# Optimization experiments

Measured on AMD Instinct MI355X. Metric: run time of the kernel, lower is better.

## Reference

```python
import jax, jax.numpy as jnp
import numpy as np

BN_EPS = 1e-5

def conv1x1(x, w, b):
    # x: [B,C,H,W], w: [O,C], b: [O] -> [B,O,H,W]
    return jnp.einsum('bchw,oc->bohw', x, w) + b[None, :, None, None]

def setup_inputs() -> dict:
    key = jax.random.key(0)
    ks = jax.random.split(key, 12)
    B, C, H, W = 16, 256, 64, 32
    Ci = C // 2  # reduc_ratio = 2
    s_in = 1.0 / np.sqrt(C)
    s_ci = 1.0 / np.sqrt(Ci)
    return {
        'x':        jax.random.normal(ks[0], (B, C, H, W), jnp.float32),
        'w_theta':  jax.random.normal(ks[1], (Ci, C), jnp.float32) * s_in,
        'b_theta':  jax.random.normal(ks[2], (Ci,), jnp.float32) * 0.01,
        'w_phi':    jax.random.normal(ks[3], (Ci, C), jnp.float32) * s_in,
        'b_phi':    jax.random.normal(ks[4], (Ci,), jnp.float32) * 0.01,
        'w_g':      jax.random.normal(ks[5], (Ci, C), jnp.float32) * s_in,
        'b_g':      jax.random.normal(ks[6], (Ci,), jnp.float32) * 0.01,
        'w_out':    jax.random.normal(ks[7], (C, Ci), jnp.float32) * s_ci,
        'b_out':    jax.random.normal(ks[8], (C,), jnp.float32) * 0.01,
        'gamma':    jax.random.normal(ks[9], (C,), jnp.float32) * 0.1 + 1.0,
        'beta':     jax.random.normal(ks[10], (C,), jnp.float32) * 0.1,
        'run_mean': jax.random.normal(ks[11], (C,), jnp.float32) * 0.1,
        'run_var':  jax.random.uniform(jax.random.fold_in(key, 99), (C,), jnp.float32, 0.5, 1.5),
    }

def reference(x, w_theta, b_theta, w_phi, b_phi, w_g, b_g, w_out, b_out,
              gamma, beta, run_mean, run_var):
    B, C, H, W = x.shape
    Ci = w_theta.shape[0]
    N = H * W
    theta = conv1x1(x, w_theta, b_theta).reshape(B, Ci, N)  # [B,Ci,N]
    phi   = conv1x1(x, w_phi,   b_phi  ).reshape(B, Ci, N)  # [B,Ci,N]
    g     = conv1x1(x, w_g,     b_g    ).reshape(B, Ci, N)  # [B,Ci,N]
    # f = theta^T @ phi, normalized by N (no softmax)
    f = jnp.einsum('bcn,bcm->bnm', theta, phi) / N           # [B,N,N]
    # y = f @ g^T, back to channel-first layout
    y = jnp.einsum('bnm,bcm->bcn', f, g).reshape(B, Ci, H, W)
    w_y = conv1x1(y, w_out, b_out)                           # [B,C,H,W]
    inv = gamma / jnp.sqrt(run_var + BN_EPS)
    bn = w_y * inv[None, :, None, None] + (beta - run_mean * inv)[None, :, None, None]
    return bn + x
```

## Files before the change

kernel.cpp:

```cpp
#include <hip/hip_runtime.h>
#include <cstddef>
#include <cstdint>

typedef unsigned short ushort_t;
typedef short short8 __attribute__((ext_vector_type(8)));
typedef float f32x4 __attribute__((ext_vector_type(4)));

#define BB 16
#define CC 256
#define CI 128
#define KK3 384
#define NN 2048
#define BN_EPS 1e-5f
#define NCHUNK 8

#define OFF_W3H   0u
#define OFF_B3    49152u
#define OFF_B2    49536u
#define OFF_XHT   49792u
#define OFF_THT   4244096u
#define OFF_TPG   6341248u
#define OFF_SPART 10535552u
#define OFF_S     12632704u
#define OFF_MH    12894848u
#define WS_FLOATS 13156992u

__device__ __forceinline__ ushort_t f2bf(float f) {
  unsigned int u = __float_as_uint(f);
  u += 0x7fffu + ((u >> 16) & 1u);
  return (ushort_t)(u >> 16);
}

__device__ __forceinline__ void gl_lds16(const void* gsrc, void* ldst) {
  __builtin_amdgcn_global_load_lds(
      (const __attribute__((address_space(1))) void*)gsrc,
      (__attribute__((address_space(3))) void*)ldst, 16, 0, 0);
}

__device__ __forceinline__ void mfma_core(
    const ushort_t* gA, size_t ldA, const ushort_t* gB, size_t ldB,
    int kIters, ushort_t* ldsA, ushort_t* ldsB, f32x4 acc[4][4]) {
  const int t = threadIdx.x;
  const int wave = t >> 6, lane = t & 63;
  const int wm = wave & 1, wn = wave >> 1;
  const int l15 = lane & 15, lhi = lane >> 4;

  for (int kt = 0; kt < kIters; ++kt) {
#pragma unroll
    for (int q = 0; q < 4; ++q) {
      int row = wave * 32 + q * 8 + (lane >> 3);
      int gs = (lane & 7) ^ (row & 7);
      gl_lds16(gA + (size_t)row * ldA + gs * 8, &ldsA[(wave * 4 + q) * 512]);
    }
#pragma unroll
    for (int q = 0; q < 4; ++q) {
      int row = wave * 32 + q * 8 + (lane >> 3);
      int gs = (lane & 7) ^ (row & 7);
      gl_lds16(gB + (size_t)row * ldB + gs * 8, &ldsB[(wave * 4 + q) * 512]);
    }
    __syncthreads();
#pragma unroll
    for (int ks = 0; ks < 2; ++ks) {
      short8 af[4], bf[4];
#pragma unroll
      for (int i = 0; i < 4; ++i) {
        int rowA = wm * 64 + i * 16 + l15;
        int grA = (4 * ks + lhi) ^ (rowA & 7);
        af[i] = *(const short8*)&ldsA[rowA * 64 + grA * 8];
        int rowB = wn * 64 + i * 16 + l15;
        int grB = (4 * ks + lhi) ^ (rowB & 7);
        bf[i] = *(const short8*)&ldsB[rowB * 64 + grB * 8];
      }
#pragma unroll
      for (int i = 0; i < 4; ++i)
#pragma unroll
        for (int j = 0; j < 4; ++j)
          acc[i][j] = __builtin_amdgcn_mfma_f32_16x16x32_bf16(
              af[i], bf[j], acc[i][j], 0, 0, 0);
    }
    __syncthreads();
    gA += 64; gB += 64;
  }
}

__global__ __launch_bounds__(256) void pack_w(
    const float* __restrict__ wt, const float* __restrict__ bt,
    const float* __restrict__ wp, const float* __restrict__ bp,
    const float* __restrict__ wg, const float* __restrict__ bg,
    const float* __restrict__ b_out, const float* __restrict__ gamma,
    const float* __restrict__ beta, const float* __restrict__ run_mean,
    const float* __restrict__ run_var,
    ushort_t* __restrict__ W3h, float* __restrict__ bias3,
    float* __restrict__ bias2) {
  int gid = blockIdx.x * 256 + threadIdx.x;
  if (gid < KK3 * CC) {
    int k = gid >> 8;
    float v;
    if (k < CI)          v = wt[gid];
    else if (k < 2 * CI) v = wp[gid - CI * CC];
    else                 v = wg[gid - 2 * CI * CC];
    W3h[gid] = f2bf(v);
  }
  if (gid < KK3)
    bias3[gid] = (gid < CI) ? bt[gid] : (gid < 2 * CI ? bp[gid - CI] : bg[gid - 2 * CI]);
  if (gid < CC) {
    float inv = gamma[gid] * rsqrtf(run_var[gid] + BN_EPS);
    bias2[gid] = b_out[gid] * inv + beta[gid] - run_mean[gid] * inv;
  }
}

__global__ __launch_bounds__(256) void cast_xT(
    const float* __restrict__ x, ushort_t* __restrict__ xhT) {
  __shared__ float Xs[64][65];
  int n0 = blockIdx.x * 64, c0 = blockIdx.y * 64, b = blockIdx.z;
  int t = threadIdx.x;
  int tr = t >> 4, tc = (t & 15) * 4;
#pragma unroll
  for (int p = 0; p < 4; ++p) {
    int row = p * 16 + tr;
    float4 v = *(const float4*)&x[((size_t)b * CC + c0 + row) * NN + n0 + tc];
    Xs[row][tc] = v.x; Xs[row][tc + 1] = v.y; Xs[row][tc + 2] = v.z; Xs[row][tc + 3] = v.w;
  }
  __syncthreads();
#pragma unroll
  for (int p = 0; p < 4; ++p) {
    int j = p * 16 + tr;
    ushort4 hv;
    hv.x = f2bf(Xs[tc][j]); hv.y = f2bf(Xs[tc + 1][j]);
    hv.z = f2bf(Xs[tc + 2][j]); hv.w = f2bf(Xs[tc + 3][j]);
    *(ushort4*)&xhT[((size_t)b * NN + n0 + j) * CC + c0 + tc] = hv;
  }
}

__global__ __launch_bounds__(256) void k1_tpg(
    const ushort_t* __restrict__ xhT, const ushort_t* __restrict__ W3h,
    const float* __restrict__ bias3, ushort_t* __restrict__ thT,
    ushort_t* __restrict__ tpg_pg) {
  __shared__ __align__(16) ushort_t As[128 * 64], Bs[128 * 64];
  int n0 = blockIdx.x * 128, m0 = blockIdx.y * 128, b = blockIdx.z;
  f32x4 acc[4][4];
#pragma unroll
  for (int i = 0; i < 4; ++i)
#pragma unroll
    for (int j = 0; j < 4; ++j)
#pragma unroll
      for (int e = 0; e < 4; ++e) acc[i][j][e] = 0.f;

  mfma_core(xhT + ((size_t)b * NN + n0) * CC, CC,
            W3h + (size_t)m0 * CC, CC, CC / 64, As, Bs, acc);

  int t = threadIdx.x, wave = t >> 6, lane = t & 63;
  int wm = wave & 1, wn = wave >> 1, l15 = lane & 15, lhi = lane >> 4;
#pragma unroll
  for (int j = 0; j < 4; ++j) {
    int m = m0 + wn * 64 + j * 16 + l15;
    float bj = bias3[m];
#pragma unroll
    for (int i = 0; i < 4; ++i)
#pragma unroll
      for (int r = 0; r < 4; ++r) {
        int n = n0 + wm * 64 + i * 16 + 4 * lhi + r;
        ushort_t h = f2bf(acc[i][j][r] + bj);
        if (m0 == 0)
          thT[((size_t)b * NN + n) * CI + m] = h;
        else
          tpg_pg[((size_t)b * CC + (m - 128)) * NN + n] = h;
      }
  }
}

__global__ __launch_bounds__(256) void k2_S(
    const ushort_t* __restrict__ tpg_pg, float* __restrict__ S_part) {
  __shared__ __align__(16) ushort_t As[128 * 64], Bs[128 * 64];
  int chunk = blockIdx.x, b = blockIdx.y;
  int nbase = chunk * (NN / NCHUNK);
  f32x4 acc[4][4];
#pragma unroll
  for (int i = 0; i < 4; ++i)
#pragma unroll
    for (int j = 0; j < 4; ++j)
#pragma unroll
      for (int e = 0; e < 4; ++e) acc[i][j][e] = 0.f;

  mfma_core(tpg_pg + ((size_t)b * CC + CI) * NN + nbase, NN,
            tpg_pg + (size_t)b * CC * NN + nbase, NN,
            (NN / NCHUNK) / 64, As, Bs, acc);

  int t = threadIdx.x, wave = t >> 6, lane = t & 63;
  int wm = wave & 1, wn = wave >> 1, l15 = lane & 15, lhi = lane >> 4;
  float* dst = S_part + ((size_t)chunk * BB + b) * (CI * CI);
#pragma unroll
  for (int i = 0; i < 4; ++i)
#pragma unroll
    for (int j = 0; j < 4; ++j)
#pragma unroll
      for (int r = 0; r < 4; ++r) {
        int ig = wm * 64 + i * 16 + 4 * lhi + r;
        int jg = wn * 64 + j * 16 + l15;
        dst[(size_t)ig * CI + jg] = acc[i][j][r];
      }
}

__global__ __launch_bounds__(256) void k2b_reduce(
    const float* __restrict__ S_part, float* __restrict__ S) {
  int b = blockIdx.y;
  int e = blockIdx.x * 256 + threadIdx.x;
  float s = 0.f;
#pragma unroll
  for (int c = 0; c < NCHUNK; ++c)
    s += S_part[((size_t)c * BB + b) * (CI * CI) + e];
  S[(size_t)b * (CI * CI) + e] = s;
}

__global__ __launch_bounds__(256) void gemm_M(
    const float* __restrict__ S, const float* __restrict__ w_out,
    const float* __restrict__ gamma, const float* __restrict__ run_var,
    ushort_t* __restrict__ Mh) {
  __shared__ __align__(16) float Sl[128][128];
  __shared__ __align__(16) float Wl[64][128];
  int b = blockIdx.y, o0 = blockIdx.x * 64, t = threadIdx.x;
  const float* Sb = S + (size_t)b * CI * CI;
#pragma unroll 4
  for (int r = 0; r < 64; ++r) {
    int idx = r * 256 + t;
    Sl[idx >> 7][idx & 127] = Sb[idx];
  }
#pragma unroll 4
  for (int r = 0; r < 32; ++r) {
    int idx = r * 256 + t;
    Wl[idx >> 7][idx & 127] = w_out[(size_t)o0 * CI + idx];
  }
  __syncthreads();

  int tx = t & 31, ty = t >> 5;
  float acc[8][4] = {};
  for (int ci = 0; ci < 128; ++ci) {
    float4 sv = *reinterpret_cast<const float4*>(&Sl[ci][tx * 4]);
    float s[4] = {sv.x, sv.y, sv.z, sv.w};
#pragma unroll
    for (int i = 0; i < 8; ++i) {
      float w = Wl[ty * 8 + i][ci];
#pragma unroll
      for (int j = 0; j < 4; ++j) acc[i][j] += w * s[j];
    }
  }
#pragma unroll
  for (int i = 0; i < 8; ++i) {
    int o = o0 + ty * 8 + i;
    float sc = gamma[o] * rsqrtf(run_var[o] + BN_EPS) * (1.0f / (float)NN);
    ushort4 hv;
    hv.x = f2bf(acc[i][0] * sc); hv.y = f2bf(acc[i][1] * sc);
    hv.z = f2bf(acc[i][2] * sc); hv.w = f2bf(acc[i][3] * sc);
    *(ushort4*)&Mh[((size_t)b * CC + o) * CI + tx * 4] = hv;
  }
}

__global__ __launch_bounds__(256) void k4_out(
    const ushort_t* __restrict__ Mh, const ushort_t* __restrict__ thT,
    const float* __restrict__ bias2, const float* __restrict__ x,
    float* __restrict__ out) {
  __shared__ __align__(16) ushort_t As[128 * 64], Bs[128 * 64];
  int n0 = blockIdx.x * 128, o0 = blockIdx.y * 128, b = blockIdx.z;
  f32x4 acc[4][4];
#pragma unroll
  for (int i = 0; i < 4; ++i)
#pragma unroll
    for (int j = 0; j < 4; ++j)
#pragma unroll
      for (int e = 0; e < 4; ++e) acc[i][j][e] = 0.f;

  mfma_core(Mh + ((size_t)b * CC + o0) * CI, CI,
            thT + ((size_t)b * NN + n0) * CI, CI, CI / 64, As, Bs, acc);

  int t = threadIdx.x, wave = t >> 6, lane = t & 63;
  int wm = wave & 1, wn = wave >> 1, l15 = lane & 15, lhi = lane >> 4;
#pragma unroll
  for (int i = 0; i < 4; ++i)
#pragma unroll
    for (int r = 0; r < 4; ++r) {
      int o = o0 + wm * 64 + i * 16 + 4 * lhi + r;
      float bo = bias2[o];
#pragma unroll
      for (int j = 0; j < 4; ++j) {
        int n = n0 + wn * 64 + j * 16 + l15;
        size_t idx = ((size_t)b * CC + o) * NN + n;
        out[idx] = acc[i][j][r] + bo + x[idx];
      }
    }
}

extern "C" void kernel_launch(void* const* d_in, const int* in_sizes, int n_in,
                              void* d_out, int out_size, void* d_ws, size_t ws_size,
                              hipStream_t stream) {
  const float* x        = (const float*)d_in[0];
  const float* w_theta  = (const float*)d_in[1];
  const float* b_theta  = (const float*)d_in[2];
  const float* w_phi    = (const float*)d_in[3];
  const float* b_phi    = (const float*)d_in[4];
  const float* w_g      = (const float*)d_in[5];
  const float* b_g      = (const float*)d_in[6];
  const float* w_out    = (const float*)d_in[7];
  const float* b_out    = (const float*)d_in[8];
  const float* gamma    = (const float*)d_in[9];
  const float* beta     = (const float*)d_in[10];
  const float* run_mean = (const float*)d_in[11];
  const float* run_var  = (const float*)d_in[12];
  float* out = (float*)d_out;
  float* ws  = (float*)d_ws;

  if (ws_size < (size_t)WS_FLOATS * sizeof(float)) return;

  ushort_t* W3h    = (ushort_t*)(ws + OFF_W3H);
  float*    bias3  = ws + OFF_B3;
  float*    bias2  = ws + OFF_B2;
  ushort_t* xhT    = (ushort_t*)(ws + OFF_XHT);
  ushort_t* thT    = (ushort_t*)(ws + OFF_THT);
  ushort_t* tpg_pg = (ushort_t*)(ws + OFF_TPG);
  float*    S_part = ws + OFF_SPART;
  float*    S      = ws + OFF_S;
  ushort_t* Mh     = (ushort_t*)(ws + OFF_MH);

  pack_w<<<dim3((KK3 * CC + 255) / 256), 256, 0, stream>>>(
      w_theta, b_theta, w_phi, b_phi, w_g, b_g,
      b_out, gamma, beta, run_mean, run_var, W3h, bias3, bias2);
  cast_xT<<<dim3(NN / 64, CC / 64, BB), 256, 0, stream>>>(x, xhT);
  k1_tpg<<<dim3(NN / 128, KK3 / 128, BB), 256, 0, stream>>>(
      xhT, W3h, bias3, thT, tpg_pg);
  k2_S<<<dim3(NCHUNK, BB), 256, 0, stream>>>(tpg_pg, S_part);
  k2b_reduce<<<dim3(CI * CI / 256, BB), 256, 0, stream>>>(S_part, S);
  gemm_M<<<dim3(4, BB), 256, 0, stream>>>(S, w_out, gamma, run_var, Mh);
  k4_out<<<dim3(NN / 128, CC / 128, BB), 256, 0, stream>>>(
      Mh, thT, bias2, x, out);
}
```

Measured before the change: 173.0 us.

## Reassociate non-local block into per-batch Gram matrix and fused 256x256 operator

Since there is no softmax, the output is linear in x. The code computes the per-batch Gram matrix x·xᵀ (256x256) and a channel sum vector, then builds a per-batch 256x256 operator P = E·Wg·G·Wθᵀ·Wφ. Bias terms are folded in algebraically through the helper vectors q, w1, eg, v1, v2 and sq. The final pass becomes a single GEMM of P against the bf16 transposed x, replacing the separate theta/phi/g projection and the 2048-long intermediates. This trades the large projection GEMM and its traffic for more small launches, atomics and extra bf16 rounding in the chained products, which could hurt accuracy.

```diff
diff --git a/kernel.cpp b/kernel.cpp
--- a/kernel.cpp
+++ b/kernel.cpp
@@ -9,26 +9,41 @@
 #define BB 16
 #define CC 256
 #define CI 128
-#define KK3 384
 #define NN 2048
 #define BN_EPS 1e-5f
-#define NCHUNK 8
-
-#define OFF_W3H   0u
-#define OFF_B3    49152u
-#define OFF_B2    49536u
-#define OFF_XHT   49792u
-#define OFF_THT   4244096u
-#define OFF_TPG   6341248u
-#define OFF_SPART 10535552u
-#define OFF_S     12632704u
-#define OFF_MH    12894848u
-#define WS_FLOATS 13156992u
+#define NCH 4
+
+#define OFF_EH    0u
+#define OFF_WGT   16384u
+#define OFF_WFT   32768u
+#define OFF_WTT   49152u
+#define OFF_LH    65536u
+#define OFF_RT    98304u
+#define OFF_Q     131072u
+#define OFF_W1    131328u
+#define OFF_EG    131584u
+#define OFF_BB2   131840u
+#define OFF_BFBT  132096u
+#define OFF_S     132112u
+#define OFF_V1    136208u
+#define OFF_V2    140304u
+#define OFF_SQ    144400u
+#define OFF_BIASP 144416u
+#define OFF_GH    148512u
+#define OFF_TH    672800u
+#define OFF_PH    1197088u
+#define OFF_XH    1721376u
+#define OFF_XHT   5915680u
+#define OFF_GP    10109984u
+#define WS_FLOATS 14304288u
 
 __device__ __forceinline__ ushort_t f2bf(float f) {
   unsigned int u = __float_as_uint(f);
   u += 0x7fffu + ((u >> 16) & 1u);
   return (ushort_t)(u >> 16);
+}
+__device__ __forceinline__ float bf2f(ushort_t h) {
+  return __uint_as_float((unsigned int)h << 16);
 }
 
 __device__ __forceinline__ void gl_lds16(const void* gsrc, void* ldst) {
@@ -83,34 +98,83 @@
   }
 }
 
-__global__ __launch_bounds__(256) void pack_w(
-    const float* __restrict__ wt, const float* __restrict__ bt,
-    const float* __restrict__ wp, const float* __restrict__ bp,
-    const float* __restrict__ wg, const float* __restrict__ bg,
-    const float* __restrict__ b_out, const float* __restrict__ gamma,
-    const float* __restrict__ beta, const float* __restrict__ run_mean,
-    const float* __restrict__ run_var,
-    ushort_t* __restrict__ W3h, float* __restrict__ bias3,
+#define ACC_INIT(acc) \
+  _Pragma("unroll") for (int i_ = 0; i_ < 4; ++i_) \
+  _Pragma("unroll") for (int j_ = 0; j_ < 4; ++j_) \
+  _Pragma("unroll") for (int e_ = 0; e_ < 4; ++e_) acc[i_][j_][e_] = 0.f;
+
+__device__ __forceinline__ void store_bf16_D(
+    f32x4 acc[4][4], ushort_t* D, int ldd, int m0, int n0) {
+  int t = threadIdx.x, wave = t >> 6, lane = t & 63;
+  int wm = wave & 1, wn = wave >> 1, l15 = lane & 15, lhi = lane >> 4;
+#pragma unroll
+  for (int i = 0; i < 4; ++i)
+#pragma unroll
+    for (int j = 0; j < 4; ++j)
+#pragma unroll
+      for (int r = 0; r < 4; ++r) {
+        int a = m0 + wm * 64 + i * 16 + 4 * lhi + r;
+        int bc = n0 + wn * 64 + j * 16 + l15;
+        D[(size_t)a * ldd + bc] = f2bf(acc[i][j][r]);
+      }
+}
+
+__global__ __launch_bounds__(256) void pack(
+    const float* __restrict__ wg, const float* __restrict__ wp,
+    const float* __restrict__ wt, const float* __restrict__ wout,
+    const float* __restrict__ gamma, const float* __restrict__ run_var,
+    const float* __restrict__ b_out, const float* __restrict__ beta,
+    const float* __restrict__ run_mean,
+    ushort_t* __restrict__ Eh, ushort_t* __restrict__ WgT,
+    ushort_t* __restrict__ WfT, ushort_t* __restrict__ WtT,
     float* __restrict__ bias2) {
   int gid = blockIdx.x * 256 + threadIdx.x;
-  if (gid < KK3 * CC) {
-    int k = gid >> 8;
-    float v;
-    if (k < CI)          v = wt[gid];
-    else if (k < 2 * CI) v = wp[gid - CI * CC];
-    else                 v = wg[gid - 2 * CI * CC];
-    W3h[gid] = f2bf(v);
-  }
-  if (gid < KK3)
-    bias3[gid] = (gid < CI) ? bt[gid] : (gid < 2 * CI ? bp[gid - CI] : bg[gid - 2 * CI]);
-  if (gid < CC) {
-    float inv = gamma[gid] * rsqrtf(run_var[gid] + BN_EPS);
-    bias2[gid] = b_out[gid] * inv + beta[gid] - run_mean[gid] * inv;
-  }
-}
-
-__global__ __launch_bounds__(256) void cast_xT(
-    const float* __restrict__ x, ushort_t* __restrict__ xhT) {
+  if (gid < 4 * 32768) {
+    int which = gid >> 15, idx = gid & 32767;
+    int c = idx >> 7, j = idx & 127;
+    if (which == 0) {
+      float inv = gamma[c] * rsqrtf(run_var[c] + BN_EPS);
+      Eh[idx] = f2bf(inv * (1.0f / (float)NN) * wout[idx]);
+    } else {
+      const float* src = (which == 1) ? wg : (which == 2) ? wp : wt;
+      ushort_t* dst = (which == 1) ? WgT : (which == 2) ? WfT : WtT;
+      dst[idx] = f2bf(src[(size_t)j * CC + c]);
+    }
+  } else if (gid < 4 * 32768 + CC) {
+    int o = gid - 4 * 32768;
+    float inv = gamma[o] * rsqrtf(run_var[o] + BN_EPS);
+    bias2[o] = b_out[o] * inv + beta[o] - run_mean[o] * inv;
+  }
+}
+
+__global__ __launch_bounds__(256) void pack2(
+    const float* __restrict__ wp, const float* __restrict__ wt,
+    const float* __restrict__ wout, const float* __restrict__ bt,
+    const float* __restrict__ bp, const float* __restrict__ bg,
+    const float* __restrict__ gamma, const float* __restrict__ run_var,
+    float* __restrict__ q, float* __restrict__ w1, float* __restrict__ eg,
+    float* __restrict__ bfbt) {
+  int t = threadIdx.x;
+  float aq = 0.f, aw = 0.f;
+  for (int j = 0; j < CI; ++j) {
+    aq += wp[(size_t)j * CC + t] * bt[j];
+    aw += wt[(size_t)j * CC + t] * bp[j];
+  }
+  q[t] = aq; w1[t] = aw;
+  float inv = gamma[t] * rsqrtf(run_var[t] + BN_EPS);
+  float s2 = 0.f;
+  for (int i = 0; i < CI; ++i) s2 += wout[(size_t)t * CI + i] * bg[i];
+  eg[t] = inv * (1.0f / (float)NN) * s2;
+  if (t == 0) {
+    float d = 0.f;
+    for (int j = 0; j < CI; ++j) d += bp[j] * bt[j];
+    *bfbt = d;
+  }
+}
+
+__global__ __launch_bounds__(256) void cast_x(
+    const float* __restrict__ x, ushort_t* __restrict__ xhT,
+    ushort_t* __restrict__ xh, float* __restrict__ s) {
   __shared__ float Xs[64][65];
   int n0 = blockIdx.x * 64, c0 = blockIdx.y * 64, b = blockIdx.z;
   int t = threadIdx.x;
@@ -130,148 +194,156 @@
     hv.z = f2bf(Xs[tc + 2][j]); hv.w = f2bf(Xs[tc + 3][j]);
     *(ushort4*)&xhT[((size_t)b * NN + n0 + j) * CC + c0 + tc] = hv;
   }
-}
-
-__global__ __launch_bounds__(256) void k1_tpg(
-    const ushort_t* __restrict__ xhT, const ushort_t* __restrict__ W3h,
-    const float* __restrict__ bias3, ushort_t* __restrict__ thT,
-    ushort_t* __restrict__ tpg_pg) {
-  __shared__ __align__(16) ushort_t As[128 * 64], Bs[128 * 64];
-  int n0 = blockIdx.x * 128, m0 = blockIdx.y * 128, b = blockIdx.z;
-  f32x4 acc[4][4];
-#pragma unroll
-  for (int i = 0; i < 4; ++i)
-#pragma unroll
-    for (int j = 0; j < 4; ++j)
-#pragma unroll
-      for (int e = 0; e < 4; ++e) acc[i][j][e] = 0.f;
-
-  mfma_core(xhT + ((size_t)b * NN + n0) * CC, CC,
-            W3h + (size_t)m0 * CC, CC, CC / 64, As, Bs, acc);
-
+  {
+    int row = t >> 2, cg = (t & 3) * 16;
+    size_t base = ((size_t)b * CC + c0 + row) * NN + n0 + cg;
+#pragma unroll
+    for (int e = 0; e < 4; ++e) {
+      ushort4 hv;
+      hv.x = f2bf(Xs[row][cg + 4 * e]);     hv.y = f2bf(Xs[row][cg + 4 * e + 1]);
+      hv.z = f2bf(Xs[row][cg + 4 * e + 2]); hv.w = f2bf(Xs[row][cg + 4 * e + 3]);
+      *(ushort4*)&xh[base + 4 * e] = hv;
+    }
+  }
+  if (t < 64) {
+    float p = 0.f;
+    for (int j2 = 0; j2 < 64; ++j2) p += Xs[t][j2];
+    atomicAdd(&s[(size_t)b * CC + c0 + t], p);
+  }
+}
+
+__global__ __launch_bounds__(256) void gemm_k128(
+    const ushort_t* __restrict__ A, const ushort_t* __restrict__ B,
+    ushort_t* __restrict__ D) {
+  __shared__ __align__(16) ushort_t As[8192], Bs[8192];
+  int n0 = blockIdx.x * 128, m0 = blockIdx.y * 128;
+  f32x4 acc[4][4]; ACC_INIT(acc);
+  mfma_core(A + (size_t)m0 * 128, 128, B + (size_t)n0 * 128, 128, 2, As, Bs, acc);
+  store_bf16_D(acc, D, CC, m0, n0);
+}
+
+__global__ __launch_bounds__(256) void k_G(
+    const ushort_t* __restrict__ xh, float* __restrict__ G_part) {
+  __shared__ __align__(16) ushort_t As[8192], Bs[8192];
+  int ch = blockIdx.x, ij = blockIdx.y, b = blockIdx.z;
+  int ti = ij >> 1, tj = ij & 1;
+  f32x4 acc[4][4]; ACC_INIT(acc);
+  mfma_core(xh + ((size_t)b * CC + ti * 128) * NN + ch * (NN / NCH), NN,
+            xh + ((size_t)b * CC + tj * 128) * NN + ch * (NN / NCH), NN,
+            (NN / NCH) / 64, As, Bs, acc);
+  float* dst = G_part + ((size_t)ch * BB + b) * (CC * CC);
   int t = threadIdx.x, wave = t >> 6, lane = t & 63;
   int wm = wave & 1, wn = wave >> 1, l15 = lane & 15, lhi = lane >> 4;
 #pragma unroll
-  for (int j = 0; j < 4; ++j) {
-    int m = m0 + wn * 64 + j * 16 + l15;
-    float bj = bias3[m];
-#pragma unroll
-    for (int i = 0; i < 4; ++i)
+  for (int i = 0; i < 4; ++i)
+#pragma unroll
+    for (int j = 0; j < 4; ++j)
 #pragma unroll
       for (int r = 0; r < 4; ++r) {
-        int n = n0 + wm * 64 + i * 16 + 4 * lhi + r;
-        ushort_t h = f2bf(acc[i][j][r] + bj);
-        if (m0 == 0)
-          thT[((size_t)b * NN + n) * CI + m] = h;
-        else
-          tpg_pg[((size_t)b * CC + (m - 128)) * NN + n] = h;
+        int a = ti * 128 + wm * 64 + i * 16 + 4 * lhi + r;
+        int bc = tj * 128 + wn * 64 + j * 16 + l15;
+        dst[(size_t)a * CC + bc] = acc[i][j][r];
       }
-  }
-}
-
-__global__ __launch_bounds__(256) void k2_S(
-    const ushort_t* __restrict__ tpg_pg, float* __restrict__ S_part) {
-  __shared__ __align__(16) ushort_t As[128 * 64], Bs[128 * 64];
-  int chunk = blockIdx.x, b = blockIdx.y;
-  int nbase = chunk * (NN / NCHUNK);
-  f32x4 acc[4][4];
-#pragma unroll
-  for (int i = 0; i < 4; ++i)
-#pragma unroll
-    for (int j = 0; j < 4; ++j)
-#pragma unroll
-      for (int e = 0; e < 4; ++e) acc[i][j][e] = 0.f;
-
-  mfma_core(tpg_pg + ((size_t)b * CC + CI) * NN + nbase, NN,
-            tpg_pg + (size_t)b * CC * NN + nbase, NN,
-            (NN / NCHUNK) / 64, As, Bs, acc);
-
+}
+
+__global__ __launch_bounds__(256) void g_red(
+    const float* __restrict__ G_part, ushort_t* __restrict__ Gh) {
+  int b = blockIdx.y;
+  int e = blockIdx.x * 256 + threadIdx.x;
+  float v = 0.f;
+#pragma unroll
+  for (int c = 0; c < NCH; ++c)
+    v += G_part[((size_t)c * BB + b) * (CC * CC) + e];
+  Gh[(size_t)b * (CC * CC) + e] = f2bf(v);
+}
+
+__global__ __launch_bounds__(256) void k_s(
+    const ushort_t* __restrict__ Lh, const ushort_t* __restrict__ Rt,
+    const float* __restrict__ s, const float* __restrict__ q,
+    float* __restrict__ v1, float* __restrict__ v2, float* __restrict__ sq) {
+  __shared__ float sl[256], red[256];
+  int b = blockIdx.x, t = threadIdx.x;
+  sl[t] = s[(size_t)b * CC + t];
+  __syncthreads();
+  float a1 = 0.f, a2 = 0.f;
+  for (int c = 0; c < CC; ++c) {
+    a1 += bf2f(Lh[(size_t)t * CC + c]) * sl[c];
+    a2 += bf2f(Rt[(size_t)t * CC + c]) * sl[c];
+  }
+  v1[(size_t)b * CC + t] = a1;
+  v2[(size_t)b * CC + t] = a2;
+  red[t] = sl[t] * q[t];
+  __syncthreads();
+  for (int st = 128; st > 0; st >>= 1) {
+    if (t < st) red[t] += red[t + st];
+    __syncthreads();
+  }
+  if (t == 0) sq[b] = red[0];
+}
+
+__global__ __launch_bounds__(256) void c1(
+    const ushort_t* __restrict__ Lh, const ushort_t* __restrict__ Gh,
+    ushort_t* __restrict__ Th) {
+  __shared__ __align__(16) ushort_t As[8192], Bs[8192];
+  int n0 = blockIdx.x * 128, m0 = blockIdx.y * 128, b = blockIdx.z;
+  f32x4 acc[4][4]; ACC_INIT(acc);
+  mfma_core(Lh + (size_t)m0 * CC, CC,
+            Gh + (size_t)b * (CC * CC) + (size_t)n0 * CC, CC, 4, As, Bs, acc);
+  store_bf16_D(acc, Th + (size_t)b * (CC * CC), CC, m0, n0);
+}
+
+__global__ __launch_bounds__(256) void c2(
+    const ushort_t* __restrict__ Th, const ushort_t* __restrict__ Rt,
+    const float* __restrict__ v1, const float* __restrict__ v2,
+    const float* __restrict__ eg, const float* __restrict__ w1,
+    ushort_t* __restrict__ Ph) {
+  __shared__ __align__(16) ushort_t As[8192], Bs[8192];
+  int n0 = blockIdx.x * 128, m0 = blockIdx.y * 128, b = blockIdx.z;
+  f32x4 acc[4][4]; ACC_INIT(acc);
+  mfma_core(Th + (size_t)b * (CC * CC) + (size_t)m0 * CC, CC,
+            Rt + (size_t)n0 * CC, CC, 4, As, Bs, acc);
+  ushort_t* D = Ph + (size_t)b * (CC * CC);
   int t = threadIdx.x, wave = t >> 6, lane = t & 63;
   int wm = wave & 1, wn = wave >> 1, l15 = lane & 15, lhi = lane >> 4;
-  float* dst = S_part + ((size_t)chunk * BB + b) * (CI * CI);
 #pragma unroll
   for (int i = 0; i < 4; ++i)
 #pragma unroll
-    for (int j = 0; j < 4; ++j)
-#pragma unroll
-      for (int r = 0; r < 4; ++r) {
-        int ig = wm * 64 + i * 16 + 4 * lhi + r;
-        int jg = wn * 64 + j * 16 + l15;
-        dst[(size_t)ig * CI + jg] = acc[i][j][r];
+    for (int r = 0; r < 4; ++r) {
+      int o = m0 + wm * 64 + i * 16 + 4 * lhi + r;
+      float vo = v1[(size_t)b * CC + o] + (float)NN * eg[o];
+      float eo = eg[o];
+#pragma unroll
+      for (int j = 0; j < 4; ++j) {
+        int c = n0 + wn * 64 + j * 16 + l15;
+        float val = acc[i][j][r] + eo * v2[(size_t)b * CC + c] + vo * w1[c];
+        D[(size_t)o * CC + c] = f2bf(val);
       }
-}
-
-__global__ __launch_bounds__(256) void k2b_reduce(
-    const float* __restrict__ S_part, float* __restrict__ S) {
-  int b = blockIdx.y;
-  int e = blockIdx.x * 256 + threadIdx.x;
-  float s = 0.f;
-#pragma unroll
-  for (int c = 0; c < NCHUNK; ++c)
-    s += S_part[((size_t)c * BB + b) * (CI * CI) + e];
-  S[(size_t)b * (CI * CI) + e] = s;
-}
-
-__global__ __launch_bounds__(256) void gemm_M(
-    const float* __restrict__ S, const float* __restrict__ w_out,
-    const float* __restrict__ gamma, const float* __restrict__ run_var,
-    ushort_t* __restrict__ Mh) {
-  __shared__ __align__(16) float Sl[128][128];
-  __shared__ __align__(16) float Wl[64][128];
-  int b = blockIdx.y, o0 = blockIdx.x * 64, t = threadIdx.x;
-  const float* Sb = S + (size_t)b * CI * CI;
-#pragma unroll 4
-  for (int r = 0; r < 64; ++r) {
-    int idx = r * 256 + t;
-    Sl[idx >> 7][idx & 127] = Sb[idx];
-  }
-#pragma unroll 4
-  for (int r = 0; r < 32; ++r) {
-    int idx = r * 256 + t;
-    Wl[idx >> 7][idx & 127] = w_out[(size_t)o0 * CI + idx];
-  }
-  __syncthreads();
-
-  int tx = t & 31, ty = t >> 5;
-  float acc[8][4] = {};
-  for (int ci = 0; ci < 128; ++ci) {
-    float4 sv = *reinterpret_cast<const float4*>(&Sl[ci][tx * 4]);
-    float s[4] = {sv.x, sv.y, sv.z, sv.w};
-#pragma unroll
-    for (int i = 0; i < 8; ++i) {
-      float w = Wl[ty * 8 + i][ci];
-#pragma unroll
-      for (int j = 0; j < 4; ++j) acc[i][j] += w * s[j];
-    }
-  }
-#pragma unroll
-  for (int i = 0; i < 8; ++i) {
-    int o = o0 + ty * 8 + i;
-    float sc = gamma[o] * rsqrtf(run_var[o] + BN_EPS) * (1.0f / (float)NN);
-    ushort4 hv;
-    hv.x = f2bf(acc[i][0] * sc); hv.y = f2bf(acc[i][1] * sc);
-    hv.z = f2bf(acc[i][2] * sc); hv.w = f2bf(acc[i][3] * sc);
-    *(ushort4*)&Mh[((size_t)b * CC + o) * CI + tx * 4] = hv;
-  }
-}
-
-__global__ __launch_bounds__(256) void k4_out(
-    const ushort_t* __restrict__ Mh, const ushort_t* __restrict__ thT,
-    const float* __restrict__ bias2, const float* __restrict__ x,
+    }
+}
+
+__global__ __launch_bounds__(256) void k_bias(
+    const ushort_t* __restrict__ Th, const float* __restrict__ q,
+    const float* __restrict__ eg, const float* __restrict__ v1,
+    const float* __restrict__ sq, const float* __restrict__ bfbt,
+    const float* __restrict__ bias2, float* __restrict__ biasp) {
+  int b = blockIdx.x, o = threadIdx.x;
+  const ushort_t* Trow = Th + (size_t)b * (CC * CC) + (size_t)o * CC;
+  float a = 0.f;
+  for (int k = 0; k < CC; ++k) a += bf2f(Trow[k]) * q[k];
+  biasp[(size_t)b * CC + o] =
+      a + eg[o] * sq[b] + (v1[(size_t)b * CC + o] + (float)NN * eg[o]) * (*bfbt)
+      + bias2[o];
+}
+
+__global__ __launch_bounds__(256) void k_out(
+    const ushort_t* __restrict__ Ph, const ushort_t* __restrict__ xhT,
+    const float* __restrict__ biasp, const float* __restrict__ x,
     float* __restrict__ out) {
-  __shared__ __align__(16) ushort_t As[128 * 64], Bs[128 * 64];
+  __shared__ __align__(16) ushort_t As[8192], Bs[8192];
   int n0 = blockIdx.x * 128, o0 = blockIdx.y * 128, b = blockIdx.z;
-  f32x4 acc[4][4];
-#pragma unroll
-  for (int i = 0; i < 4; ++i)
-#pragma unroll
-    for (int j = 0; j < 4; ++j)
-#pragma unroll
-      for (int e = 0; e < 4; ++e) acc[i][j][e] = 0.f;
-
-  mfma_core(Mh + ((size_t)b * CC + o0) * CI, CI,
-            thT + ((size_t)b * NN + n0) * CI, CI, CI / 64, As, Bs, acc);
-
+  f32x4 acc[4][4]; ACC_INIT(acc);
+  mfma_core(Ph + (size_t)b * (CC * CC) + (size_t)o0 * CC, CC,
+            xhT + ((size_t)b * NN + n0) * CC, CC, 4, As, Bs, acc);
   int t = threadIdx.x, wave = t >> 6, lane = t & 63;
   int wm = wave & 1, wn = wave >> 1, l15 = lane & 15, lhi = lane >> 4;
 #pragma unroll
@@ -279,7 +351,7 @@
 #pragma unroll
     for (int r = 0; r < 4; ++r) {
       int o = o0 + wm * 64 + i * 16 + 4 * lhi + r;
-      float bo = bias2[o];
+      float bo = biasp[(size_t)b * CC + o];
 #pragma unroll
       for (int j = 0; j < 4; ++j) {
         int n = n0 + wn * 64 + j * 16 + l15;
@@ -310,25 +382,42 @@
 
   if (ws_size < (size_t)WS_FLOATS * sizeof(float)) return;
 
-  ushort_t* W3h    = (ushort_t*)(ws + OFF_W3H);
-  float*    bias3  = ws + OFF_B3;
-  float*    bias2  = ws + OFF_B2;
-  ushort_t* xhT    = (ushort_t*)(ws + OFF_XHT);
-  ushort_t* thT    = (ushort_t*)(ws + OFF_THT);
-  ushort_t* tpg_pg = (ushort_t*)(ws + OFF_TPG);
-  float*    S_part = ws + OFF_SPART;
-  float*    S      = ws + OFF_S;
-  ushort_t* Mh     = (ushort_t*)(ws + OFF_MH);
-
-  pack_w<<<dim3((KK3 * CC + 255) / 256), 256, 0, stream>>>(
-      w_theta, b_theta, w_phi, b_phi, w_g, b_g,
-      b_out, gamma, beta, run_mean, run_var, W3h, bias3, bias2);
-  cast_xT<<<dim3(NN / 64, CC / 64, BB), 256, 0, stream>>>(x, xhT);
-  k1_tpg<<<dim3(NN / 128, KK3 / 128, BB), 256, 0, stream>>>(
-      xhT, W3h, bias3, thT, tpg_pg);
-  k2_S<<<dim3(NCHUNK, BB), 256, 0, stream>>>(tpg_pg, S_part);
-  k2b_reduce<<<dim3(CI * CI / 256, BB), 256, 0, stream>>>(S_part, S);
-  gemm_M<<<dim3(4, BB), 256, 0, stream>>>(S, w_out, gamma, run_var, Mh);
-  k4_out<<<dim3(NN / 128, CC / 128, BB), 256, 0, stream>>>(
-      Mh, thT, bias2, x, out);
-}
+  ushort_t* Eh   = (ushort_t*)(ws + OFF_EH);
+  ushort_t* WgT  = (ushort_t*)(ws + OFF_WGT);
+  ushort_t* WfT  = (ushort_t*)(ws + OFF_WFT);
+  ushort_t* WtT  = (ushort_t*)(ws + OFF_WTT);
+  ushort_t* Lh   = (ushort_t*)(ws + OFF_LH);
+  ushort_t* Rt   = (ushort_t*)(ws + OFF_RT);
+  float*    q    = ws + OFF_Q;
+  float*    w1   = ws + OFF_W1;
+  float*    eg   = ws + OFF_EG;
+  float*    bias2= ws + OFF_BB2;
+  float*    bfbt = ws + OFF_BFBT;
+  float*    s    = ws + OFF_S;
+  float*    v1   = ws + OFF_V1;
+  float*    v2   = ws + OFF_V2;
+  float*    sq   = ws + OFF_SQ;
+  float*    biasp= ws + OFF_BIASP;
+  ushort_t* Gh   = (ushort_t*)(ws + OFF_GH);
+  ushort_t* Th   = (ushort_t*)(ws + OFF_TH);
+  ushort_t* Ph   = (ushort_t*)(ws + OFF_PH);
+  ushort_t* xh   = (ushort_t*)(ws + OFF_XH);
+  ushort_t* xhT  = (ushort_t*)(ws + OFF_XHT);
+  float*    Gp   = ws + OFF_GP;
+
+  pack<<<dim3(513), 256, 0, stream>>>(w_g, w_phi, w_theta, w_out, gamma, run_var,
+                                      b_out, beta, run_mean, Eh, WgT, WfT, WtT, bias2);
+  pack2<<<dim3(1), 256, 0, stream>>>(w_phi, w_theta, w_out, b_theta, b_phi, b_g,
+                                     gamma, run_var, q, w1, eg, bfbt);
+  hipMemsetAsync(s, 0, (size_t)BB * CC * sizeof(float), stream);
+  cast_x<<<dim3(NN / 64, CC / 64, BB), 256, 0, stream>>>(x, xhT, xh, s);
+  gemm_k128<<<dim3(2, 2), 256, 0, stream>>>(Eh, WgT, Lh);
+  gemm_k128<<<dim3(2, 2), 256, 0, stream>>>(WtT, WfT, Rt);
+  k_G<<<dim3(NCH, 4, BB), 256, 0, stream>>>(xh, Gp);
+  g_red<<<dim3(CC * CC / 256, BB), 256, 0, stream>>>(Gp, Gh);
+  k_s<<<dim3(BB), 256, 0, stream>>>(Lh, Rt, s, q, v1, v2, sq);
+  c1<<<dim3(2, 2, BB), 256, 0, stream>>>(Lh, Gh, Th);
+  c2<<<dim3(2, 2, BB), 256, 0, stream>>>(Th, Rt, v1, v2, eg, w1, Ph);
+  k_bias<<<dim3(BB), 256, 0, stream>>>(Th, q, eg, v1, sq, bfbt, bias2, biasp);
+  k_out<<<dim3(NN / 128, CC / 128, BB), 256, 0, stream>>>(Ph, xhT, biasp, x, out);
+}
```

After: 207.1 us. 1.2x slower.
